# Optimization experiments

Hardware: AMD Instinct MI355X
Metric: run time of the kernel (lower is better)

The kernel has to match this reference:

```python
import jax, jax.numpy as jnp
import numpy as np
from jax import lax

DIM = 64
HEADS = 4
B, Q, V = 8, 128, 128


def _modrelu(z, b):
    m = jnp.abs(z)
    return z * (jax.nn.relu(m + b) / (m + 1e-5))


def _eunn_unitary(h, th1, ph1, th2, ph2, om):
    # tunable-style EUNN, capacity 2: even-pair rotations, odd-pair rotations, diagonal phase
    d = h.shape[-1]
    # layer 1: pairs (0,1),(2,3),...
    hp = h.reshape(*h.shape[:-1], d // 2, 2)
    a, b = hp[..., 0], hp[..., 1]
    c1, s1, e1 = jnp.cos(th1), jnp.sin(th1), jnp.exp(1j * ph1)
    h = jnp.stack([e1 * (c1 * a - s1 * b), s1 * a + c1 * b], -1).reshape(h.shape)
    # layer 2: pairs (1,2),(3,4),...,(d-3,d-2); endpoints pass through
    mid = h[..., 1:d - 1].reshape(*h.shape[:-1], d // 2 - 1, 2)
    a, b = mid[..., 0], mid[..., 1]
    c2, s2, e2 = jnp.cos(th2), jnp.sin(th2), jnp.exp(1j * ph2)
    mid2 = jnp.stack([e2 * (c2 * a - s2 * b), s2 * a + c2 * b], -1).reshape(*h.shape[:-1], d - 2)
    h = jnp.concatenate([h[..., :1], mid2, h[..., d - 1:]], -1)
    return h * jnp.exp(1j * om)


def _forward(queries, values, U_re, U_im, bias, theta1, phi1, theta2, phi2, omega, W_dense, b_dense):
    Bq, Qq, d = queries.shape
    Vv = values.shape[1]
    # quadratic (query, value) expansion -> [B*Q, V, 2d]
    dq = jnp.broadcast_to(queries[:, :, None, :], (Bq, Qq, Vv, d))
    dv = jnp.broadcast_to(values[:, None, :, :], (Bq, Qq, Vv, d))
    x = jnp.concatenate([dq, dv], -1).reshape(Bq * Qq, Vv, 2 * d)
    U = (U_re + 1j * U_im)  # [H, 2d, d] complex input kernel per head
    Ux = jnp.einsum('nvi,hij->hvnj', x.astype(jnp.complex64), U)  # [H, V, N, d]

    def run_head(Ux_h, t1, p1, t2, p2, om, bh):
        def step(h, u):
            h2 = _modrelu(_eunn_unitary(h, t1, p1, t2, p2, om) + u, bh)
            return h2, None
        h0 = jnp.zeros(Ux_h.shape[1:], dtype=jnp.complex64)  # [N, d]
        hT, _ = lax.scan(step, h0, Ux_h)
        return hT  # final state, as Keras RNN with return_sequences=False

    outs = jax.vmap(run_head)(Ux, theta1, phi1, theta2, phi2, omega, bias)  # [H, N, d]
    acc = jnp.real(outs).transpose(1, 0, 2).reshape(Bq * Qq, HEADS * d)
    y = acc @ W_dense + b_dense
    return y.reshape(Bq, Qq, d)


def setup_inputs() -> dict:
    key = jax.random.key(0)
    ks = jax.random.split(key, 12)
    pi = np.pi
    return {
        'queries': jax.random.normal(ks[0], (B, Q, DIM), jnp.float32),
        'values': jax.random.normal(ks[1], (B, V, DIM), jnp.float32),
        'U_re': jax.random.normal(ks[2], (HEADS, 2 * DIM, DIM), jnp.float32) * (1.0 / np.sqrt(2 * DIM)),
        'U_im': jax.random.normal(ks[3], (HEADS, 2 * DIM, DIM), jnp.float32) * (1.0 / np.sqrt(2 * DIM)),
        'bias': jax.random.normal(ks[4], (HEADS, DIM), jnp.float32) * 0.01,
        'theta1': jax.random.uniform(ks[5], (HEADS, DIM // 2), jnp.float32, -pi, pi),
        'phi1': jax.random.uniform(ks[6], (HEADS, DIM // 2), jnp.float32, -pi, pi),
        'theta2': jax.random.uniform(ks[7], (HEADS, DIM // 2 - 1), jnp.float32, -pi, pi),
        'phi2': jax.random.uniform(ks[8], (HEADS, DIM // 2 - 1), jnp.float32, -pi, pi),
        'omega': jax.random.uniform(ks[9], (HEADS, DIM), jnp.float32, -pi, pi),
        'W_dense': jax.random.normal(ks[10], (HEADS * DIM, DIM), jnp.float32) * (1.0 / np.sqrt(HEADS * DIM)),
        'b_dense': jnp.zeros((DIM,), jnp.float32),
    }


def reference(queries, values, U_re, U_im, bias, theta1, phi1, theta2, phi2, omega, W_dense, b_dense):
    return _forward(queries, values, U_re, U_im, bias, theta1, phi1, theta2, phi2, omega, W_dense, b_dense)
```

## Files before the change

kernel.cpp:

```cpp
#include <hip/hip_runtime.h>
#include <math.h>

#define DIM 64
#define HEADS 4
#define BB 8
#define QQ 128
#define VV 128
#define NN (BB*QQ)

typedef float f2 __attribute__((ext_vector_type(2)));

template <int CTRL>
__device__ __forceinline__ float dppf(float x) {
    return __int_as_float(__builtin_amdgcn_update_dpp(
        0, __float_as_int(x), CTRL, 0xF, 0xF, true));
}
#define SWAP1 0xB1
#define WSHR1 0x138
#define WSHL1 0x130

__global__ __launch_bounds__(256) void k_av(const float* __restrict__ values,
                                            const float* __restrict__ U_re,
                                            const float* __restrict__ U_im,
                                            f2* __restrict__ Av) {
    int tid = blockIdx.x * blockDim.x + threadIdx.x;
    int w = tid >> 6;
    int j = tid & 63;
    int h = w >> 9;
    int r0 = (w & 511) << 1;
    const float* vrow = values + r0 * DIM;
    const float* ur = U_re + (h * 2 * DIM + DIM) * DIM + j;
    const float* ui = U_im + (h * 2 * DIM + DIM) * DIM + j;
    f2 a0 = 0.f, a1 = 0.f;
    #pragma unroll 8
    for (int i = 0; i < DIM; ++i) {
        f2 u; u.x = ur[i * DIM]; u.y = ui[i * DIM];
        a0 += vrow[i] * u;
        a1 += vrow[DIM + i] * u;
    }
    f2* out = Av + (h * 1024 + r0) * DIM + j;
    out[0] = a0; out[DIM] = a1;
}

__global__ __launch_bounds__(256, 4) void k_rnn_dense(
        const float* __restrict__ queries,
        const float* __restrict__ U_re,
        const float* __restrict__ U_im,
        const float* __restrict__ bias,
        const float* __restrict__ theta1,
        const float* __restrict__ phi1,
        const float* __restrict__ theta2,
        const float* __restrict__ phi2,
        const float* __restrict__ omega,
        const f2* __restrict__ Av,
        const float* __restrict__ W_dense,
        const float* __restrict__ b_dense,
        float* __restrict__ y) {
    int n = blockIdx.x;
    int t = threadIdx.x;
    int h = t >> 6;
    int j = t & 63;
    int b = n >> 7;

    int k1 = j >> 1;
    float th1 = theta1[h * 32 + k1], ph1 = phi1[h * 32 + k1];
    float C1 = cosf(th1), s1v = sinf(th1);
    float S1, E1r, E1i;
    if ((j & 1) == 0) { S1 = -s1v; E1r = cosf(ph1); E1i = sinf(ph1); }
    else              { S1 =  s1v; E1r = 1.f;       E1i = 0.f;       }

    float C2, SL, SR, p2r, p2i;
    if (j == 0 || j == 63) {
        C2 = 1.f; SL = 0.f; SR = 0.f; p2r = 1.f; p2i = 0.f;
    } else {
        int k2 = (j - 1) >> 1;
        float th2 = theta2[h * 31 + k2], ph2 = phi2[h * 31 + k2];
        float c2 = cosf(th2), s2 = sinf(th2);
        if (j & 1) { C2 = c2; SL = -s2; SR = 0.f; p2r = cosf(ph2); p2i = sinf(ph2); }
        else       { C2 = c2; SR =  s2; SL = 0.f; p2r = 1.f;       p2i = 0.f;       }
    }
    float om = omega[h * 64 + j];
    float eor = cosf(om), eoi = sinf(om);
    float PHr = p2r * eor - p2i * eoi;
    float PHi = p2r * eoi + p2i * eor;
    float bj = bias[h * 64 + j];

    const float* qrow = queries + n * DIM;
    const float* ur = U_re + (h * 2 * DIM) * DIM + j;
    const float* ui = U_im + (h * 2 * DIM) * DIM + j;
    float uqr = 0.f, uqi = 0.f;
    #pragma unroll 8
    for (int i = 0; i < DIM; ++i) {
        float a = qrow[i];
        uqr = fmaf(a, ur[i * DIM], uqr);
        uqi = fmaf(a, ui[i * DIM], uqi);
    }

    float hr = 0.f, hi = 0.f;
    auto step = [&](f2 av) {
        float uvr = uqr + av.x;
        float uvi = uqi + av.y;
        float pr = dppf<SWAP1>(hr), pi = dppf<SWAP1>(hi);
        float tpr = fmaf(C1, hr, S1 * pr);
        float tpi = fmaf(C1, hi, S1 * pi);
        float Tr = fmaf(E1r, tpr, -E1i * tpi);
        float Ti = fmaf(E1r, tpi,  E1i * tpr);
        float Lr = dppf<WSHL1>(Tr), Li = dppf<WSHL1>(Ti);
        float Rr = dppf<WSHR1>(Tr), Ri = dppf<WSHR1>(Ti);
        float spr = fmaf(C2, Tr, fmaf(SL, Lr, SR * Rr));
        float spi = fmaf(C2, Ti, fmaf(SL, Li, SR * Ri));
        float zr = fmaf(PHr, spr, fmaf(-PHi, spi, uvr));
        float zi = fmaf(PHr, spi, fmaf( PHi, spr, uvi));
        float q2 = fmaf(zr, zr, fmaf(zi, zi, 1e-10f));
        float rs = __builtin_amdgcn_rsqf(q2);
        float sc = fmaxf(fmaf(bj, rs, 1.f), 0.f);
        hr = zr * sc; hi = zi * sc;
    };

    const f2* p = Av + (h * 1024 + b * 128) * DIM + j;

    f2 buf[8], nxt[8];
    #pragma unroll
    for (int k = 0; k < 8; ++k) buf[k] = p[k * DIM];

    for (int vb = 0; vb < VV; vb += 8) {
        const f2* pn = p + ((vb < VV - 8) ? 8 * DIM : 0);
        #pragma unroll
        for (int k = 0; k < 8; ++k) nxt[k] = pn[k * DIM];
        p = pn;
        #pragma unroll
        for (int k = 0; k < 8; ++k) step(buf[k]);
        #pragma unroll
        for (int k = 0; k < 8; ++k) buf[k] = nxt[k];
    }

    __shared__ float s_acc[HEADS * DIM];
    __shared__ float s_part[256];
    s_acc[h * 64 + j] = hr;
    __syncthreads();

    {
        int qq = t >> 6, jj = t & 63;
        const float* Wp = W_dense + (qq * 64) * DIM + jj;
        const float* ap = &s_acc[qq * 64];
        float part = 0.f;
        #pragma unroll 8
        for (int k = 0; k < 64; ++k)
            part = fmaf(ap[k], Wp[k * DIM], part);
        s_part[t] = part;
    }
    __syncthreads();
    if (t < 64) {
        y[n * DIM + t] = b_dense[t] + s_part[t] + s_part[64 + t]
                       + s_part[128 + t] + s_part[192 + t];
    }
}

extern "C" void kernel_launch(void* const* d_in, const int* in_sizes, int n_in,
                              void* d_out, int out_size, void* d_ws, size_t ws_size,
                              hipStream_t stream) {
    const float* queries = (const float*)d_in[0];
    const float* values  = (const float*)d_in[1];
    const float* U_re    = (const float*)d_in[2];
    const float* U_im    = (const float*)d_in[3];
    const float* bias    = (const float*)d_in[4];
    const float* theta1  = (const float*)d_in[5];
    const float* phi1    = (const float*)d_in[6];
    const float* theta2  = (const float*)d_in[7];
    const float* phi2    = (const float*)d_in[8];
    const float* omega   = (const float*)d_in[9];
    const float* W_dense = (const float*)d_in[10];
    const float* b_dense = (const float*)d_in[11];
    float* y = (float*)d_out;

    f2* Av = (f2*)d_ws;

    k_av<<<512, 256, 0, stream>>>(values, U_re, U_im, Av);
    k_rnn_dense<<<1024, 256, 0, stream>>>(queries, U_re, U_im, bias, theta1,
                                          phi1, theta2, phi2, omega, Av,
                                          W_dense, b_dense, y);
}
```

Measured before the change: 113.5 us.

## Give each lane a complex pair and pack two query rows per wavefront

Each lane now owns two adjacent complex state elements (one rotation pair), so the first-layer rotation is done in registers without a DPP swap. Each 64-lane wavefront handles two sequence rows (32 lanes each), which halves the block count and loads the precomputed value projection as float4. The dense epilogue is reorganised to produce two output rows per block. This trades more registers per thread and a dropped occupancy hint for fewer cross-lane ops and twice the work per lane.

```diff
diff --git a/kernel.cpp b/kernel.cpp
--- a/kernel.cpp
+++ b/kernel.cpp
@@ -9,13 +9,13 @@
 #define NN (BB*QQ)
 
 typedef float f2 __attribute__((ext_vector_type(2)));
+typedef float f4 __attribute__((ext_vector_type(4)));
 
 template <int CTRL>
 __device__ __forceinline__ float dppf(float x) {
     return __int_as_float(__builtin_amdgcn_update_dpp(
         0, __float_as_int(x), CTRL, 0xF, 0xF, true));
 }
-#define SWAP1 0xB1
 #define WSHR1 0x138
 #define WSHL1 0x130
 
@@ -42,7 +42,7 @@
     out[0] = a0; out[DIM] = a1;
 }
 
-__global__ __launch_bounds__(256, 4) void k_rnn_dense(
+__global__ __launch_bounds__(256) void k_rnn_dense(
         const float* __restrict__ queries,
         const float* __restrict__ U_re,
         const float* __restrict__ U_im,
@@ -52,107 +52,128 @@
         const float* __restrict__ theta2,
         const float* __restrict__ phi2,
         const float* __restrict__ omega,
-        const f2* __restrict__ Av,
+        const float* __restrict__ Av,
         const float* __restrict__ W_dense,
         const float* __restrict__ b_dense,
         float* __restrict__ y) {
-    int n = blockIdx.x;
+    int b = blockIdx.x >> 6;
+    int q = blockIdx.x & 63;
     int t = threadIdx.x;
     int h = t >> 6;
-    int j = t & 63;
-    int b = n >> 7;
-
-    int k1 = j >> 1;
-    float th1 = theta1[h * 32 + k1], ph1 = phi1[h * 32 + k1];
-    float C1 = cosf(th1), s1v = sinf(th1);
-    float S1, E1r, E1i;
-    if ((j & 1) == 0) { S1 = -s1v; E1r = cosf(ph1); E1i = sinf(ph1); }
-    else              { S1 =  s1v; E1r = 1.f;       E1i = 0.f;       }
-
-    float C2, SL, SR, p2r, p2i;
-    if (j == 0 || j == 63) {
-        C2 = 1.f; SL = 0.f; SR = 0.f; p2r = 1.f; p2i = 0.f;
-    } else {
-        int k2 = (j - 1) >> 1;
-        float th2 = theta2[h * 31 + k2], ph2 = phi2[h * 31 + k2];
-        float c2 = cosf(th2), s2 = sinf(th2);
-        if (j & 1) { C2 = c2; SL = -s2; SR = 0.f; p2r = cosf(ph2); p2i = sinf(ph2); }
-        else       { C2 = c2; SR =  s2; SL = 0.f; p2r = 1.f;       p2i = 0.f;       }
-    }
-    float om = omega[h * 64 + j];
-    float eor = cosf(om), eoi = sinf(om);
-    float PHr = p2r * eor - p2i * eoi;
-    float PHi = p2r * eoi + p2i * eor;
-    float bj = bias[h * 64 + j];
-
-    const float* qrow = queries + n * DIM;
-    const float* ur = U_re + (h * 2 * DIM) * DIM + j;
-    const float* ui = U_im + (h * 2 * DIM) * DIM + j;
-    float uqr = 0.f, uqi = 0.f;
+    int l = t & 63;
+    int k = l & 31;
+    int n0 = b * 128 + q;
+    int n1 = n0 + 64;
+    int myrow = (l < 32) ? n0 : n1;
+
+    float th1 = theta1[h * 32 + k], ph1 = phi1[h * 32 + k];
+    float C1 = cosf(th1), S1 = sinf(th1), nS1 = -S1;
+    float E1r = cosf(ph1), E1i = sinf(ph1), nE1i = -E1i;
+
+    float C2b, nS2b, e2r, e2i;
+    if (k < 31) {
+        float th2 = theta2[h * 31 + k], ph2 = phi2[h * 31 + k];
+        C2b = cosf(th2); nS2b = -sinf(th2);
+        e2r = cosf(ph2); e2i = sinf(ph2);
+    } else { C2b = 1.f; nS2b = 0.f; e2r = 1.f; e2i = 0.f; }
+    float C2a, SRa;
+    if (k > 0) {
+        float th2p = theta2[h * 31 + (k - 1)];
+        C2a = cosf(th2p); SRa = sinf(th2p);
+    } else { C2a = 1.f; SRa = 0.f; }
+
+    float oma = omega[h * 64 + 2 * k], omb = omega[h * 64 + 2 * k + 1];
+    float PHar = cosf(oma), PHai = sinf(oma), nPHai = -PHai;
+    float obr = cosf(omb), obi = sinf(omb);
+    float PHbr = e2r * obr - e2i * obi;
+    float PHbi = e2r * obi + e2i * obr;
+    float nPHbi = -PHbi;
+    float bja = bias[h * 64 + 2 * k], bjb = bias[h * 64 + 2 * k + 1];
+
+    const float* qp = queries + myrow * DIM;
+    const f2* urp = (const f2*)(U_re + (h * 2 * DIM) * DIM + 2 * k);
+    const f2* uip = (const f2*)(U_im + (h * 2 * DIM) * DIM + 2 * k);
+    float uqar = 0.f, uqai = 0.f, uqbr = 0.f, uqbi = 0.f;
     #pragma unroll 8
     for (int i = 0; i < DIM; ++i) {
-        float a = qrow[i];
-        uqr = fmaf(a, ur[i * DIM], uqr);
-        uqi = fmaf(a, ui[i * DIM], uqi);
-    }
-
-    float hr = 0.f, hi = 0.f;
-    auto step = [&](f2 av) {
-        float uvr = uqr + av.x;
-        float uvi = uqi + av.y;
-        float pr = dppf<SWAP1>(hr), pi = dppf<SWAP1>(hi);
-        float tpr = fmaf(C1, hr, S1 * pr);
-        float tpi = fmaf(C1, hi, S1 * pi);
-        float Tr = fmaf(E1r, tpr, -E1i * tpi);
-        float Ti = fmaf(E1r, tpi,  E1i * tpr);
-        float Lr = dppf<WSHL1>(Tr), Li = dppf<WSHL1>(Ti);
-        float Rr = dppf<WSHR1>(Tr), Ri = dppf<WSHR1>(Ti);
-        float spr = fmaf(C2, Tr, fmaf(SL, Lr, SR * Rr));
-        float spi = fmaf(C2, Ti, fmaf(SL, Li, SR * Ri));
-        float zr = fmaf(PHr, spr, fmaf(-PHi, spi, uvr));
-        float zi = fmaf(PHr, spi, fmaf( PHi, spr, uvi));
-        float q2 = fmaf(zr, zr, fmaf(zi, zi, 1e-10f));
-        float rs = __builtin_amdgcn_rsqf(q2);
-        float sc = fmaxf(fmaf(bj, rs, 1.f), 0.f);
-        hr = zr * sc; hi = zi * sc;
+        float qv = qp[i];
+        f2 wr = urp[i * (DIM / 2)];
+        f2 wi = uip[i * (DIM / 2)];
+        uqar = fmaf(qv, wr.x, uqar); uqbr = fmaf(qv, wr.y, uqbr);
+        uqai = fmaf(qv, wi.x, uqai); uqbi = fmaf(qv, wi.y, uqbi);
+    }
+
+    float ar = 0.f, ai = 0.f, br = 0.f, bi = 0.f;
+    auto step = [&](f4 av) {
+        float uvar = uqar + av.x, uvai = uqai + av.y;
+        float uvbr = uqbr + av.z, uvbi = uqbi + av.w;
+        float tar = C1 * ar; tar = fmaf(nS1, br, tar);
+        float tai = C1 * ai; tai = fmaf(nS1, bi, tai);
+        float Tar = fmaf(E1r, tar, nE1i * tai);
+        float Tai = fmaf(E1r, tai, E1i * tar);
+        float Tbr = fmaf(S1, ar, C1 * br);
+        float Tbi = fmaf(S1, ai, C1 * bi);
+        float Lar = dppf<WSHL1>(Tar), Lai = dppf<WSHL1>(Tai);
+        float Rbr = dppf<WSHR1>(Tbr), Rbi = dppf<WSHR1>(Tbi);
+        float bppr = C2b * Tbr; bppr = fmaf(nS2b, Lar, bppr);
+        float bppi = C2b * Tbi; bppi = fmaf(nS2b, Lai, bppi);
+        float appr = C2a * Tar; appr = fmaf(SRa, Rbr, appr);
+        float appi = C2a * Tai; appi = fmaf(SRa, Rbi, appi);
+        float zar = fmaf(PHar, appr, fmaf(nPHai, appi, uvar));
+        float zai = fmaf(PHar, appi, fmaf(PHai, appr, uvai));
+        float zbr = fmaf(PHbr, bppr, fmaf(nPHbi, bppi, uvbr));
+        float zbi = fmaf(PHbr, bppi, fmaf(PHbi, bppr, uvbi));
+        float q2a = fmaf(zar, zar, fmaf(zai, zai, 1e-10f));
+        float rsa = __builtin_amdgcn_rsqf(q2a);
+        float sca = fmaxf(fmaf(bja, rsa, 1.f), 0.f);
+        ar = zar * sca; ai = zai * sca;
+        float q2b = fmaf(zbr, zbr, fmaf(zbi, zbi, 1e-10f));
+        float rsb = __builtin_amdgcn_rsqf(q2b);
+        float scb = fmaxf(fmaf(bjb, rsb, 1.f), 0.f);
+        br = zbr * scb; bi = zbi * scb;
     };
 
-    const f2* p = Av + (h * 1024 + b * 128) * DIM + j;
-
-    f2 buf[8], nxt[8];
+    const f4* p = (const f4*)Av + (h * 1024 + b * 128) * 32 + k;
+
+    f4 buf[4], nxt[4];
     #pragma unroll
-    for (int k = 0; k < 8; ++k) buf[k] = p[k * DIM];
-
-    for (int vb = 0; vb < VV; vb += 8) {
-        const f2* pn = p + ((vb < VV - 8) ? 8 * DIM : 0);
+    for (int m = 0; m < 4; ++m) buf[m] = p[m * 32];
+
+    for (int vb = 0; vb < VV; vb += 4) {
+        const f4* pn = p + ((vb < VV - 4) ? 4 * 32 : 0);
         #pragma unroll
-        for (int k = 0; k < 8; ++k) nxt[k] = pn[k * DIM];
+        for (int m = 0; m < 4; ++m) nxt[m] = pn[m * 32];
         p = pn;
         #pragma unroll
-        for (int k = 0; k < 8; ++k) step(buf[k]);
+        for (int m = 0; m < 4; ++m) step(buf[m]);
         #pragma unroll
-        for (int k = 0; k < 8; ++k) buf[k] = nxt[k];
-    }
-
-    __shared__ float s_acc[HEADS * DIM];
+        for (int m = 0; m < 4; ++m) buf[m] = nxt[m];
+    }
+
+    __shared__ float s_acc[2][HEADS * DIM];
     __shared__ float s_part[256];
-    s_acc[h * 64 + j] = hr;
+    {
+        int c = l >> 5;
+        s_acc[c][h * 64 + 2 * k]     = ar;
+        s_acc[c][h * 64 + 2 * k + 1] = br;
+    }
     __syncthreads();
 
     {
-        int qq = t >> 6, jj = t & 63;
-        const float* Wp = W_dense + (qq * 64) * DIM + jj;
-        const float* ap = &s_acc[qq * 64];
+        int r = t >> 7, hf = (t >> 6) & 1, jj = t & 63;
+        const float* Wp = W_dense + (hf * 128) * DIM + jj;
+        const float* ap = &s_acc[r][hf * 128];
         float part = 0.f;
         #pragma unroll 8
-        for (int k = 0; k < 64; ++k)
-            part = fmaf(ap[k], Wp[k * DIM], part);
+        for (int kk = 0; kk < 128; ++kk)
+            part = fmaf(ap[kk], Wp[kk * DIM], part);
         s_part[t] = part;
     }
     __syncthreads();
-    if (t < 64) {
-        y[n * DIM + t] = b_dense[t] + s_part[t] + s_part[64 + t]
-                       + s_part[128 + t] + s_part[192 + t];
+    if (t < 128) {
+        int r = t >> 6, jj = t & 63;
+        y[(n0 + r * 64) * DIM + jj] =
+            b_dense[jj] + s_part[r * 128 + jj] + s_part[r * 128 + 64 + jj];
     }
 }
 
@@ -176,7 +197,7 @@
     f2* Av = (f2*)d_ws;
 
     k_av<<<512, 256, 0, stream>>>(values, U_re, U_im, Av);
-    k_rnn_dense<<<1024, 256, 0, stream>>>(queries, U_re, U_im, bias, theta1,
-                                          phi1, theta2, phi2, omega, Av,
-                                          W_dense, b_dense, y);
-}
+    k_rnn_dense<<<512, 256, 0, stream>>>(queries, U_re, U_im, bias, theta1,
+                                         phi1, theta2, phi2, omega, (const float*)Av,
+                                         W_dense, b_dense, y);
+}
```

After: 117.8 us. 3.8% more time.
